# Kernel optimization log

Measured on AMD Instinct MI355X. Metric: run time of the kernel, lower is better.

## Reference

```python
import jax, jax.numpy as jnp
import numpy as np

N_A, N_S, D, H = 100000, 50000, 256, 128
E_AA, E_SS, E_SA = 800000, 400000, 800000


def setup_inputs() -> dict:
    key = jax.random.key(0)
    ks = jax.random.split(key, 13)
    s = 0.05
    return {
        "x_article": jax.random.normal(ks[0], (N_A, D), dtype=jnp.float32),
        "x_software": jax.random.normal(ks[1], (N_S, D), dtype=jnp.float32),
        "ei_aa": jax.random.randint(ks[2], (2, E_AA), 0, N_A, dtype=jnp.int32),
        "ei_ss": jax.random.randint(ks[3], (2, E_SS), 0, N_S, dtype=jnp.int32),
        "sa_src": jax.random.randint(ks[4], (E_SA,), 0, N_S, dtype=jnp.int32),
        "sa_dst": jax.random.randint(ks[5], (E_SA,), 0, N_A, dtype=jnp.int32),
        # GCNConv article->article: weight [D,H], bias [H]
        "W_aa": jax.random.normal(ks[6], (D, H), dtype=jnp.float32) * s,
        "b_aa": jnp.zeros((H,), dtype=jnp.float32),
        # GCNConv software->software
        "W_ss": jax.random.normal(ks[7], (D, H), dtype=jnp.float32) * s,
        "b_ss": jnp.zeros((H,), dtype=jnp.float32),
        # SAGEConv software->article: lin_l (neighbor, with bias), lin_r (root, no bias)
        "W_sa_l": jax.random.normal(ks[8], (D, H), dtype=jnp.float32) * s,
        "b_sa_l": jnp.zeros((H,), dtype=jnp.float32),
        "W_sa_r": jax.random.normal(ks[9], (D, H), dtype=jnp.float32) * s,
    }


def _gcn_conv(x, src, dst, W, b, n):
    # PyG GCNConv: transform, add self-loops (weight 1), symmetric norm, scatter-add
    h = x @ W  # [n, H]
    loops = jnp.arange(n, dtype=src.dtype)
    s = jnp.concatenate([src, loops])
    d = jnp.concatenate([dst, loops])
    w = jnp.ones(s.shape[0], dtype=h.dtype)
    deg = jax.ops.segment_sum(w, d, num_segments=n)  # in-degree incl. self-loop
    dinv = jnp.where(deg > 0, jax.lax.rsqrt(deg), 0.0)
    norm = dinv[s] * dinv[d]  # [E+n]
    out = jax.ops.segment_sum(h[s] * norm[:, None], d, num_segments=n)
    return out + b


def _sage_conv(x_src, x_dst, src, dst, W_l, b_l, W_r, n_dst):
    # PyG SAGEConv (mean aggr): lin_l(mean_neighbors) + lin_r(x_dst)
    msum = jax.ops.segment_sum(x_src[src], dst, num_segments=n_dst)  # [n_dst, D]
    cnt = jax.ops.segment_sum(jnp.ones_like(dst, dtype=x_src.dtype), dst, num_segments=n_dst)
    mean = msum / jnp.maximum(cnt, 1.0)[:, None]
    return mean @ W_l + b_l + x_dst @ W_r


def reference(x_article, x_software, ei_aa, ei_ss, sa_src, sa_dst,
              W_aa, b_aa, W_ss, b_ss, W_sa_l, b_sa_l, W_sa_r):
    gcn_art = _gcn_conv(x_article, ei_aa[0], ei_aa[1], W_aa, b_aa, N_A)
    gcn_soft = _gcn_conv(x_software, ei_ss[0], ei_ss[1], W_ss, b_ss, N_S)
    sage_art = _sage_conv(x_software, x_article, sa_src, sa_dst, W_sa_l, b_sa_l, W_sa_r, N_A)
    # HeteroConv aggr='mean' over relations per dst type, then per-type relu
    art = jax.nn.relu((gcn_art + sage_art) * 0.5)
    soft = jax.nn.relu(gcn_soft)
    return art, soft
```

## Files before the change

kernel.cpp:

```cpp
#include <hip/hip_runtime.h>

typedef short short8 __attribute__((ext_vector_type(8)));
typedef float float4v __attribute__((ext_vector_type(4)));
typedef __bf16 bf16x8 __attribute__((ext_vector_type(8)));

#define NA_ 100000
#define NS_ 50000
#define EAA_ 800000
#define ESS_ 400000
#define ESA_ 800000
#define POOLE_ (EAA_ + ESA_ + ESS_)
#define NNODES_ (NA_ + NA_ + NS_)
#define SCAN_BLOCKS_ 62
#define NPAD_ (SCAN_BLOCKS_ * 4096)

static __device__ __forceinline__ float b2f(short s) {
  unsigned int u = ((unsigned int)(unsigned short)s) << 16;
  return __builtin_bit_cast(float, u);
}
static __device__ __forceinline__ short f2b(float f) {
  unsigned int u = __builtin_bit_cast(unsigned int, f);
  u = u + 0x7FFFu + ((u >> 16) & 1u);
  return (short)(u >> 16);
}

__global__ void cvt_k(const float* __restrict__ x, short* __restrict__ y, int n8) {
  int i = blockIdx.x * 256 + threadIdx.x;
  if (i >= n8) return;
  const float* xp = x + (long)i * 8;
  float4v a0 = *(const float4v*)xp;
  float4v a1 = *(const float4v*)(xp + 4);
  short8 r;
#pragma unroll
  for (int j = 0; j < 4; ++j) {
    r[j] = f2b(a0[j]);
    r[4 + j] = f2b(a1[j]);
  }
  *(short8*)&y[(long)i * 8] = r;
}

__global__ void transpose_all_k(const float* __restrict__ W0, const float* __restrict__ W1,
                                const float* __restrict__ W2, const float* __restrict__ W3,
                                short* __restrict__ T0, short* __restrict__ T1,
                                short* __restrict__ T2, short* __restrict__ T3) {
  int tid = blockIdx.x * 256 + threadIdx.x;
  int which = tid >> 15, r = tid & 32767;
  const float* W = which == 0 ? W0 : which == 1 ? W1 : which == 2 ? W2 : W3;
  short* T = which == 0 ? T0 : which == 1 ? T1 : which == 2 ? T2 : T3;
  int k = r >> 7, n = r & 127;
  T[n * 256 + k] = f2b(W[k * 128 + n]);
}

#define LDN 136
__global__ __launch_bounds__(256) void gemm_k(const short* __restrict__ A,
                                              const short* __restrict__ Wt,
                                              short* __restrict__ C, int M) {
  __shared__ short lds[128 * LDN];
  int tid = threadIdx.x;
  int wave = tid >> 6, lane = tid & 63;
  int l16 = lane & 15, lq = lane >> 4;
  int rowBase = blockIdx.x * 256 + wave * 64;

  float4v acc[4][8];
#pragma unroll
  for (int rt = 0; rt < 4; ++rt)
#pragma unroll
    for (int ct = 0; ct < 8; ++ct) acc[rt][ct] = (float4v){0.f, 0.f, 0.f, 0.f};

  for (int phase = 0; phase < 2; ++phase) {
    int kg = phase * 128;
    __syncthreads();
    for (int idx = tid; idx < 128 * 16; idx += 256) {
      int n = idx >> 4, c = idx & 15;
      *(short8*)&lds[n * LDN + c * 8] = *(const short8*)&Wt[n * 256 + kg + c * 8];
    }
    __syncthreads();
#pragma unroll
    for (int ks = 0; ks < 4; ++ks) {
      int k0 = kg + ks * 32;
      short8 af[4];
#pragma unroll
      for (int rt = 0; rt < 4; ++rt) {
        int row = rowBase + rt * 16 + l16;
        if (row >= M) row = M - 1;
        af[rt] = *(const short8*)&A[(long)row * 256 + k0 + lq * 8];
      }
#pragma unroll
      for (int ct = 0; ct < 8; ++ct) {
        short8 bfg = *(const short8*)&lds[(ct * 16 + l16) * LDN + ks * 32 + lq * 8];
#pragma unroll
        for (int rt = 0; rt < 4; ++rt) {
          acc[rt][ct] = __builtin_amdgcn_mfma_f32_16x16x32_bf16(
              __builtin_bit_cast(bf16x8, af[rt]), __builtin_bit_cast(bf16x8, bfg),
              acc[rt][ct], 0, 0, 0);
        }
      }
    }
  }
#pragma unroll
  for (int rt = 0; rt < 4; ++rt) {
    int r0 = rowBase + rt * 16 + lq * 4;
#pragma unroll
    for (int ct = 0; ct < 8; ++ct) {
      int col = ct * 16 + l16;
#pragma unroll
      for (int r = 0; r < 4; ++r) {
        int row = r0 + r;
        if (row < M) C[(long)row * 128 + col] = f2b(acc[rt][ct][r]);
      }
    }
  }
}

__global__ void count_all_k(const int* __restrict__ dst_aa, const int* __restrict__ sa_dst,
                            const int* __restrict__ dst_ss, int* __restrict__ cnt) {
  int i = blockIdx.x * 256 + threadIdx.x;
  if (i < EAA_) atomicAdd(&cnt[dst_aa[i]], 1);
  else if (i < EAA_ + ESA_) atomicAdd(&cnt[NA_ + sa_dst[i - EAA_]], 1);
  else if (i < POOLE_) atomicAdd(&cnt[2 * NA_ + dst_ss[i - EAA_ - ESA_]], 1);
}

__global__ void scanA_k(const int* __restrict__ in, int* __restrict__ part,
                        int* __restrict__ bsums) {
  __shared__ int lds[256];
  int t = threadIdx.x, b = blockIdx.x;
  int base = b * 4096 + t * 16;
  int v[16];
  int run = 0;
#pragma unroll
  for (int j = 0; j < 16; ++j) {
    int x = (base + j < NNODES_) ? in[base + j] : 0;
    v[j] = run;
    run += x;
  }
  lds[t] = run;
  __syncthreads();
  int incl = run;
  for (int off = 1; off < 256; off <<= 1) {
    int add = (t >= off) ? lds[t - off] : 0;
    __syncthreads();
    lds[t] += add;
    incl = lds[t];
    __syncthreads();
  }
  int excl = incl - run;
#pragma unroll
  for (int j = 0; j < 16; ++j) part[base + j] = v[j] + excl;
  if (t == 255) bsums[b] = incl;
}
__global__ void scanB_k(int* __restrict__ bsums) {
  __shared__ int lds[256];
  int t = threadIdx.x;
  int v = (t < SCAN_BLOCKS_) ? bsums[t] : 0;
  lds[t] = v;
  __syncthreads();
  int incl = v;
  for (int off = 1; off < 256; off <<= 1) {
    int add = (t >= off) ? lds[t - off] : 0;
    __syncthreads();
    lds[t] += add;
    incl = lds[t];
    __syncthreads();
  }
  if (t < SCAN_BLOCKS_) bsums[t] = incl - v;
}
__global__ void scanC_k(const int* __restrict__ part, const int* __restrict__ bsums,
                        int* __restrict__ row_ptr, int* __restrict__ cursor) {
  int t = threadIdx.x, b = blockIdx.x;
  int base = b * 4096 + t * 16;
  int sb = bsums[b];
#pragma unroll
  for (int j = 0; j < 16; ++j) {
    int val = part[base + j] + sb;
    row_ptr[base + j] = val;
    cursor[base + j] = val;
  }
}
__global__ void fill_all_k(const int* __restrict__ src_aa, const int* __restrict__ dst_aa,
                           const int* __restrict__ sa_src, const int* __restrict__ sa_dst,
                           const int* __restrict__ src_ss, const int* __restrict__ dst_ss,
                           int* __restrict__ cursor, int* __restrict__ pool) {
  int i = blockIdx.x * 256 + threadIdx.x;
  int s, node;
  if (i < EAA_) { s = src_aa[i]; node = dst_aa[i]; }
  else if (i < EAA_ + ESA_) { int j = i - EAA_; s = sa_src[j]; node = NA_ + sa_dst[j]; }
  else if (i < POOLE_) { int j = i - EAA_ - ESA_; s = src_ss[j]; node = 2 * NA_ + dst_ss[j]; }
  else return;
  int pos = atomicAdd(&cursor[node], 1);
  pool[pos] = s;
}

__global__ void norms_k(const int* __restrict__ cnt, float* __restrict__ dinv_aa,
                        float* __restrict__ dinv_ss, float* __restrict__ invc_sa) {
  int i = blockIdx.x * 256 + threadIdx.x;
  if (i < NA_) {
    dinv_aa[i] = rsqrtf((float)(cnt[i] + 1));
    invc_sa[i] = 1.0f / fmaxf((float)cnt[NA_ + i], 1.0f);
  }
  if (i < NS_) dinv_ss[i] = rsqrtf((float)(cnt[2 * NA_ + i] + 1));
}

__global__ __launch_bounds__(256) void gather_art_k(
    const short* __restrict__ h_aa, const short* __restrict__ y_sl,
    const short* __restrict__ r_a, const int* __restrict__ pool,
    const int* __restrict__ row_ptr, const float* __restrict__ dinv_aa,
    const float* __restrict__ invc_sa, const float* __restrict__ b_aa,
    const float* __restrict__ b_sal, float* __restrict__ out) {
  int wave = threadIdx.x >> 6, lane = threadIdx.x & 63;
  int d = blockIdx.x * 4 + wave;
  if (d >= NA_) return;
  int c = lane * 2;
  float dd = dinv_aa[d];

  float a0 = 0.f, a1 = 0.f;
  {
    int r0 = row_ptr[d], r1 = row_ptr[d + 1];
    for (int jj = r0; jj < r1; jj += 8) {
      int s[8];
      float m[8];
#pragma unroll
      for (int t = 0; t < 8; ++t) {
        int j = jj + t;
        int jc = (j < r1) ? j : (POOLE_ - 1);
        s[t] = pool[jc];
        m[t] = (j < r1) ? 1.f : 0.f;
      }
      short2 hv[8];
#pragma unroll
      for (int t = 0; t < 8; ++t) hv[t] = *(const short2*)&h_aa[(long)s[t] * 128 + c];
      float wv[8];
#pragma unroll
      for (int t = 0; t < 8; ++t) wv[t] = dinv_aa[s[t]] * m[t];
#pragma unroll
      for (int t = 0; t < 8; ++t) {
        float w = wv[t] * dd;
        a0 += b2f(hv[t].x) * w;
        a1 += b2f(hv[t].y) * w;
      }
    }
  }
  float s0 = 0.f, s1 = 0.f;
  {
    int r0 = row_ptr[NA_ + d], r1 = row_ptr[NA_ + d + 1];
    for (int jj = r0; jj < r1; jj += 8) {
      int s[8];
      float m[8];
#pragma unroll
      for (int t = 0; t < 8; ++t) {
        int j = jj + t;
        int jc = (j < r1) ? j : (POOLE_ - 1);
        s[t] = pool[jc];
        m[t] = (j < r1) ? 1.f : 0.f;
      }
      short2 yv[8];
#pragma unroll
      for (int t = 0; t < 8; ++t) yv[t] = *(const short2*)&y_sl[(long)s[t] * 128 + c];
#pragma unroll
      for (int t = 0; t < 8; ++t) {
        s0 += b2f(yv[t].x) * m[t];
        s1 += b2f(yv[t].y) * m[t];
      }
    }
  }
  float ic = invc_sa[d];
  float d2 = dd * dd;
  short2 hv = *(const short2*)&h_aa[(long)d * 128 + c];
  short2 rv = *(const short2*)&r_a[(long)d * 128 + c];
  float2 ba = *(const float2*)&b_aa[c];
  float2 bl = *(const float2*)&b_sal[c];
  float o0 = 0.5f * ((a0 + b2f(hv.x) * d2 + ba.x) + (s0 * ic + bl.x + b2f(rv.x)));
  float o1 = 0.5f * ((a1 + b2f(hv.y) * d2 + ba.y) + (s1 * ic + bl.y + b2f(rv.y)));
  float2 res = make_float2(fmaxf(o0, 0.f), fmaxf(o1, 0.f));
  *(float2*)&out[(long)d * 128 + c] = res;
}

__global__ __launch_bounds__(256) void gather_soft_k(
    const short* __restrict__ h_ss, const int* __restrict__ pool,
    const int* __restrict__ row_ptr, const float* __restrict__ dinv_ss,
    const float* __restrict__ b_ss, float* __restrict__ out) {
  int wave = threadIdx.x >> 6, lane = threadIdx.x & 63;
  int d = blockIdx.x * 4 + wave;
  if (d >= NS_) return;
  int c = lane * 2;
  float dd = dinv_ss[d];
  float a0 = 0.f, a1 = 0.f;
  int r0 = row_ptr[2 * NA_ + d], r1 = row_ptr[2 * NA_ + d + 1];
  for (int jj = r0; jj < r1; jj += 8) {
    int s[8];
    float m[8];
#pragma unroll
    for (int t = 0; t < 8; ++t) {
      int j = jj + t;
      int jc = (j < r1) ? j : (POOLE_ - 1);
      s[t] = pool[jc];
      m[t] = (j < r1) ? 1.f : 0.f;
    }
    short2 hv[8];
#pragma unroll
    for (int t = 0; t < 8; ++t) hv[t] = *(const short2*)&h_ss[(long)s[t] * 128 + c];
    float wv[8];
#pragma unroll
    for (int t = 0; t < 8; ++t) wv[t] = dinv_ss[s[t]] * m[t];
#pragma unroll
    for (int t = 0; t < 8; ++t) {
      float w = wv[t] * dd;
      a0 += b2f(hv[t].x) * w;
      a1 += b2f(hv[t].y) * w;
    }
  }
  float d2 = dd * dd;
  short2 hv = *(const short2*)&h_ss[(long)d * 128 + c];
  float2 bs = *(const float2*)&b_ss[c];
  float o0 = a0 + b2f(hv.x) * d2 + bs.x;
  float o1 = a1 + b2f(hv.y) * d2 + bs.y;
  float2 res = make_float2(fmaxf(o0, 0.f), fmaxf(o1, 0.f));
  *(float2*)&out[(long)d * 128 + c] = res;
}

extern "C" void kernel_launch(void* const* d_in, const int* in_sizes, int n_in,
                              void* d_out, int out_size, void* d_ws, size_t ws_size,
                              hipStream_t stream) {
  const float* x_a = (const float*)d_in[0];
  const float* x_s = (const float*)d_in[1];
  const int* ei_aa = (const int*)d_in[2];
  const int* ei_ss = (const int*)d_in[3];
  const int* sa_src = (const int*)d_in[4];
  const int* sa_dst = (const int*)d_in[5];
  const float* W_aa = (const float*)d_in[6];
  const float* b_aa = (const float*)d_in[7];
  const float* W_ss = (const float*)d_in[8];
  const float* b_ss = (const float*)d_in[9];
  const float* W_sal = (const float*)d_in[10];
  const float* b_sal = (const float*)d_in[11];
  const float* W_sar = (const float*)d_in[12];

  const int* src_aa = ei_aa;
  const int* dst_aa = ei_aa + EAA_;
  const int* src_ss = ei_ss;
  const int* dst_ss = ei_ss + ESS_;

  char* base = (char*)d_ws;
  size_t off = 0;
  auto alloc = [&](size_t bytes) {
    void* p = base + off;
    off += (bytes + 511) & ~(size_t)511;
    return p;
  };
  short* xb_a = (short*)alloc((size_t)NA_ * 256 * 2);
  short* xb_s = (short*)alloc((size_t)NS_ * 256 * 2);
  short* h_aa = (short*)alloc((size_t)NA_ * 128 * 2);
  short* h_ss = (short*)alloc((size_t)NS_ * 128 * 2);
  short* y_sl = (short*)alloc((size_t)NS_ * 128 * 2);
  short* r_a = (short*)alloc((size_t)NA_ * 128 * 2);
  int* pool = (int*)alloc((size_t)POOLE_ * 4);
  int* cnt_all = (int*)alloc((size_t)NNODES_ * 4);
  int* part = (int*)alloc((size_t)NPAD_ * 4);
  int* row_ptr = (int*)alloc((size_t)NPAD_ * 4);
  int* cursor = (int*)alloc((size_t)NPAD_ * 4);
  int* bsums = (int*)alloc(256 * 4);
  float* dinv_aa = (float*)alloc((size_t)NA_ * 4);
  float* dinv_ss = (float*)alloc((size_t)NS_ * 4);
  float* invc_sa = (float*)alloc((size_t)NA_ * 4);
  short* Wt_aa = (short*)alloc(128 * 256 * 2);
  short* Wt_ss = (short*)alloc(128 * 256 * 2);
  short* Wt_sal = (short*)alloc(128 * 256 * 2);
  short* Wt_sar = (short*)alloc(128 * 256 * 2);

  float* out_art = (float*)d_out;
  float* out_soft = (float*)d_out + (size_t)NA_ * 128;

  int gA = (NA_ + 255) / 256, gS = (NS_ + 255) / 256;

  hipMemsetAsync(cnt_all, 0, (size_t)NNODES_ * 4, stream);
  count_all_k<<<(POOLE_ + 255) / 256, 256, 0, stream>>>(dst_aa, sa_dst, dst_ss, cnt_all);
  scanA_k<<<SCAN_BLOCKS_, 256, 0, stream>>>(cnt_all, part, bsums);
  scanB_k<<<1, 256, 0, stream>>>(bsums);
  scanC_k<<<SCAN_BLOCKS_, 256, 0, stream>>>(part, bsums, row_ptr, cursor);
  fill_all_k<<<(POOLE_ + 255) / 256, 256, 0, stream>>>(src_aa, dst_aa, sa_src, sa_dst, src_ss,
                                                       dst_ss, cursor, pool);
  norms_k<<<(NA_ + 255) / 256, 256, 0, stream>>>(cnt_all, dinv_aa, dinv_ss, invc_sa);

  transpose_all_k<<<512, 256, 0, stream>>>(W_aa, W_ss, W_sal, W_sar, Wt_aa, Wt_ss, Wt_sal,
                                           Wt_sar);
  cvt_k<<<(NA_ * 32 + 255) / 256, 256, 0, stream>>>(x_a, xb_a, NA_ * 32);
  cvt_k<<<(NS_ * 32 + 255) / 256, 256, 0, stream>>>(x_s, xb_s, NS_ * 32);
  gemm_k<<<gA, 256, 0, stream>>>(xb_a, Wt_aa, h_aa, NA_);
  gemm_k<<<gA, 256, 0, stream>>>(xb_a, Wt_sar, r_a, NA_);
  gemm_k<<<gS, 256, 0, stream>>>(xb_s, Wt_ss, h_ss, NS_);
  gemm_k<<<gS, 256, 0, stream>>>(xb_s, Wt_sal, y_sl, NS_);

  gather_art_k<<<(NA_ + 3) / 4, 256, 0, stream>>>(h_aa, y_sl, r_a, pool, row_ptr, dinv_aa,
                                                  invc_sa, b_aa, b_sal, out_art);
  gather_soft_k<<<(NS_ + 3) / 4, 256, 0, stream>>>(h_ss, pool, row_ptr, dinv_ss, b_ss, out_soft);
}
```

Before: 648.4 us.

## Fuse paired GEMMs, precompute edge weights into CSR pool, drop second atomic pass

Each input matrix now goes through one GEMM kernel that computes both weight projections at once, so A is read once per node type instead of twice. CSR construction records each edge's slot from the counting atomic, so the fill pass no longer needs a second atomic cursor. It also stores a precomputed normalization weight next to each source index in an int2 pool. The norm kernel is folded into the scan, and the gather kernels read the weight straight from the pool instead of doing an extra dinv lookup per edge. The cost is a pool twice as large plus a pos array, and a GEMM tile with fewer rows per block.

```diff
diff --git a/kernel.cpp b/kernel.cpp
--- a/kernel.cpp
+++ b/kernel.cpp
@@ -51,45 +51,48 @@
   T[n * 256 + k] = f2b(W[k * 128 + n]);
 }
 
-#define LDN 136
-__global__ __launch_bounds__(256) void gemm_k(const short* __restrict__ A,
-                                              const short* __restrict__ Wt,
-                                              short* __restrict__ C, int M) {
-  __shared__ short lds[128 * LDN];
+#define LDK 72
+__global__ __launch_bounds__(256) void gemm2_k(const short* __restrict__ A,
+                                               const short* __restrict__ Wt0,
+                                               const short* __restrict__ Wt1,
+                                               short* __restrict__ C0,
+                                               short* __restrict__ C1, int M) {
+  __shared__ short lds[256 * LDK];
   int tid = threadIdx.x;
   int wave = tid >> 6, lane = tid & 63;
   int l16 = lane & 15, lq = lane >> 4;
-  int rowBase = blockIdx.x * 256 + wave * 64;
-
-  float4v acc[4][8];
-#pragma unroll
-  for (int rt = 0; rt < 4; ++rt)
-#pragma unroll
-    for (int ct = 0; ct < 8; ++ct) acc[rt][ct] = (float4v){0.f, 0.f, 0.f, 0.f};
-
-  for (int phase = 0; phase < 2; ++phase) {
-    int kg = phase * 128;
-    __syncthreads();
-    for (int idx = tid; idx < 128 * 16; idx += 256) {
-      int n = idx >> 4, c = idx & 15;
-      *(short8*)&lds[n * LDN + c * 8] = *(const short8*)&Wt[n * 256 + kg + c * 8];
-    }
-    __syncthreads();
-#pragma unroll
-    for (int ks = 0; ks < 4; ++ks) {
-      int k0 = kg + ks * 32;
-      short8 af[4];
-#pragma unroll
-      for (int rt = 0; rt < 4; ++rt) {
+  int rowBase = blockIdx.x * 128 + wave * 32;
+
+  float4v acc[2][16];
+#pragma unroll
+  for (int rt = 0; rt < 2; ++rt)
+#pragma unroll
+    for (int ct = 0; ct < 16; ++ct) acc[rt][ct] = (float4v){0.f, 0.f, 0.f, 0.f};
+
+  for (int p = 0; p < 4; ++p) {
+    int kp = p * 64;
+    __syncthreads();
+    for (int idx = tid; idx < 2048; idx += 256) {
+      int row = idx >> 3, c = idx & 7;
+      const short* Wsrc = (row < 128) ? &Wt0[row * 256] : &Wt1[(row - 128) * 256];
+      *(short8*)&lds[row * LDK + c * 8] = *(const short8*)&Wsrc[kp + c * 8];
+    }
+    __syncthreads();
+#pragma unroll
+    for (int ks = 0; ks < 2; ++ks) {
+      int k0 = kp + ks * 32;
+      short8 af[2];
+#pragma unroll
+      for (int rt = 0; rt < 2; ++rt) {
         int row = rowBase + rt * 16 + l16;
         if (row >= M) row = M - 1;
         af[rt] = *(const short8*)&A[(long)row * 256 + k0 + lq * 8];
       }
 #pragma unroll
-      for (int ct = 0; ct < 8; ++ct) {
-        short8 bfg = *(const short8*)&lds[(ct * 16 + l16) * LDN + ks * 32 + lq * 8];
-#pragma unroll
-        for (int rt = 0; rt < 4; ++rt) {
+      for (int ct = 0; ct < 16; ++ct) {
+        short8 bfg = *(const short8*)&lds[(ct * 16 + l16) * LDK + ks * 32 + lq * 8];
+#pragma unroll
+        for (int rt = 0; rt < 2; ++rt) {
           acc[rt][ct] = __builtin_amdgcn_mfma_f32_16x16x32_bf16(
               __builtin_bit_cast(bf16x8, af[rt]), __builtin_bit_cast(bf16x8, bfg),
               acc[rt][ct], 0, 0, 0);
@@ -98,11 +101,12 @@
     }
   }
 #pragma unroll
-  for (int rt = 0; rt < 4; ++rt) {
+  for (int rt = 0; rt < 2; ++rt) {
     int r0 = rowBase + rt * 16 + lq * 4;
 #pragma unroll
-    for (int ct = 0; ct < 8; ++ct) {
-      int col = ct * 16 + l16;
+    for (int ct = 0; ct < 16; ++ct) {
+      short* C = (ct < 8) ? C0 : C1;
+      int col = (ct & 7) * 16 + l16;
 #pragma unroll
       for (int r = 0; r < 4; ++r) {
         int row = r0 + r;
@@ -112,12 +116,16 @@
   }
 }
 
-__global__ void count_all_k(const int* __restrict__ dst_aa, const int* __restrict__ sa_dst,
-                            const int* __restrict__ dst_ss, int* __restrict__ cnt) {
+__global__ void count_pos_k(const int* __restrict__ dst_aa, const int* __restrict__ sa_dst,
+                            const int* __restrict__ dst_ss, int* __restrict__ cnt,
+                            int* __restrict__ pos) {
   int i = blockIdx.x * 256 + threadIdx.x;
-  if (i < EAA_) atomicAdd(&cnt[dst_aa[i]], 1);
-  else if (i < EAA_ + ESA_) atomicAdd(&cnt[NA_ + sa_dst[i - EAA_]], 1);
-  else if (i < POOLE_) atomicAdd(&cnt[2 * NA_ + dst_ss[i - EAA_ - ESA_]], 1);
+  int node;
+  if (i < EAA_) node = dst_aa[i];
+  else if (i < EAA_ + ESA_) node = NA_ + sa_dst[i - EAA_];
+  else if (i < POOLE_) node = 2 * NA_ + dst_ss[i - EAA_ - ESA_];
+  else return;
+  pos[i] = atomicAdd(&cnt[node], 1);
 }
 
 __global__ void scanA_k(const int* __restrict__ in, int* __restrict__ part,
@@ -165,75 +173,83 @@
   if (t < SCAN_BLOCKS_) bsums[t] = incl - v;
 }
 __global__ void scanC_k(const int* __restrict__ part, const int* __restrict__ bsums,
-                        int* __restrict__ row_ptr, int* __restrict__ cursor) {
+                        const int* __restrict__ cnt, int* __restrict__ row_ptr,
+                        float* __restrict__ dinv_aa, float* __restrict__ dinv_ss,
+                        float* __restrict__ invc_sa) {
   int t = threadIdx.x, b = blockIdx.x;
   int base = b * 4096 + t * 16;
   int sb = bsums[b];
 #pragma unroll
   for (int j = 0; j < 16; ++j) {
-    int val = part[base + j] + sb;
-    row_ptr[base + j] = val;
-    cursor[base + j] = val;
-  }
-}
-__global__ void fill_all_k(const int* __restrict__ src_aa, const int* __restrict__ dst_aa,
-                           const int* __restrict__ sa_src, const int* __restrict__ sa_dst,
-                           const int* __restrict__ src_ss, const int* __restrict__ dst_ss,
-                           int* __restrict__ cursor, int* __restrict__ pool) {
+    int i = base + j;
+    row_ptr[i] = part[i] + sb;
+    if (i < NA_) dinv_aa[i] = rsqrtf((float)(cnt[i] + 1));
+    else if (i < 2 * NA_) invc_sa[i - NA_] = 1.0f / fmaxf((float)cnt[i], 1.0f);
+    else if (i < NNODES_) dinv_ss[i - 2 * NA_] = rsqrtf((float)(cnt[i] + 1));
+  }
+}
+
+__global__ void fill2_k(const int* __restrict__ src_aa, const int* __restrict__ dst_aa,
+                        const int* __restrict__ sa_src, const int* __restrict__ sa_dst,
+                        const int* __restrict__ src_ss, const int* __restrict__ dst_ss,
+                        const int* __restrict__ row_ptr, const int* __restrict__ pos,
+                        const float* __restrict__ dinv_aa, const float* __restrict__ dinv_ss,
+                        const float* __restrict__ invc_sa, int2* __restrict__ pool) {
   int i = blockIdx.x * 256 + threadIdx.x;
   int s, node;
-  if (i < EAA_) { s = src_aa[i]; node = dst_aa[i]; }
-  else if (i < EAA_ + ESA_) { int j = i - EAA_; s = sa_src[j]; node = NA_ + sa_dst[j]; }
-  else if (i < POOLE_) { int j = i - EAA_ - ESA_; s = src_ss[j]; node = 2 * NA_ + dst_ss[j]; }
-  else return;
-  int pos = atomicAdd(&cursor[node], 1);
-  pool[pos] = s;
-}
-
-__global__ void norms_k(const int* __restrict__ cnt, float* __restrict__ dinv_aa,
-                        float* __restrict__ dinv_ss, float* __restrict__ invc_sa) {
-  int i = blockIdx.x * 256 + threadIdx.x;
-  if (i < NA_) {
-    dinv_aa[i] = rsqrtf((float)(cnt[i] + 1));
-    invc_sa[i] = 1.0f / fmaxf((float)cnt[NA_ + i], 1.0f);
-  }
-  if (i < NS_) dinv_ss[i] = rsqrtf((float)(cnt[2 * NA_ + i] + 1));
+  float w;
+  if (i < EAA_) {
+    s = src_aa[i];
+    int d = dst_aa[i];
+    node = d;
+    w = dinv_aa[s] * dinv_aa[d];
+  } else if (i < EAA_ + ESA_) {
+    int j = i - EAA_;
+    s = sa_src[j];
+    int d = sa_dst[j];
+    node = NA_ + d;
+    w = invc_sa[d];
+  } else if (i < POOLE_) {
+    int j = i - EAA_ - ESA_;
+    s = src_ss[j];
+    int d = dst_ss[j];
+    node = 2 * NA_ + d;
+    w = dinv_ss[s] * dinv_ss[d];
+  } else
+    return;
+  pool[row_ptr[node] + pos[i]] = make_int2(s, __builtin_bit_cast(int, w));
 }
 
 __global__ __launch_bounds__(256) void gather_art_k(
     const short* __restrict__ h_aa, const short* __restrict__ y_sl,
-    const short* __restrict__ r_a, const int* __restrict__ pool,
+    const short* __restrict__ r_a, const int2* __restrict__ pool,
     const int* __restrict__ row_ptr, const float* __restrict__ dinv_aa,
-    const float* __restrict__ invc_sa, const float* __restrict__ b_aa,
-    const float* __restrict__ b_sal, float* __restrict__ out) {
+    const float* __restrict__ b_aa, const float* __restrict__ b_sal,
+    float* __restrict__ out) {
   int wave = threadIdx.x >> 6, lane = threadIdx.x & 63;
   int d = blockIdx.x * 4 + wave;
   if (d >= NA_) return;
   int c = lane * 2;
-  float dd = dinv_aa[d];
 
   float a0 = 0.f, a1 = 0.f;
   {
     int r0 = row_ptr[d], r1 = row_ptr[d + 1];
     for (int jj = r0; jj < r1; jj += 8) {
-      int s[8];
+      int2 pv[8];
       float m[8];
 #pragma unroll
       for (int t = 0; t < 8; ++t) {
         int j = jj + t;
         int jc = (j < r1) ? j : (POOLE_ - 1);
-        s[t] = pool[jc];
+        pv[t] = pool[jc];
         m[t] = (j < r1) ? 1.f : 0.f;
       }
       short2 hv[8];
 #pragma unroll
-      for (int t = 0; t < 8; ++t) hv[t] = *(const short2*)&h_aa[(long)s[t] * 128 + c];
-      float wv[8];
-#pragma unroll
-      for (int t = 0; t < 8; ++t) wv[t] = dinv_aa[s[t]] * m[t];
+      for (int t = 0; t < 8; ++t) hv[t] = *(const short2*)&h_aa[(long)pv[t].x * 128 + c];
 #pragma unroll
       for (int t = 0; t < 8; ++t) {
-        float w = wv[t] * dd;
+        float w = __builtin_bit_cast(float, pv[t].y) * m[t];
         a0 += b2f(hv[t].x) * w;
         a1 += b2f(hv[t].y) * w;
       }
@@ -243,71 +259,69 @@
   {
     int r0 = row_ptr[NA_ + d], r1 = row_ptr[NA_ + d + 1];
     for (int jj = r0; jj < r1; jj += 8) {
-      int s[8];
+      int2 pv[8];
       float m[8];
 #pragma unroll
       for (int t = 0; t < 8; ++t) {
         int j = jj + t;
         int jc = (j < r1) ? j : (POOLE_ - 1);
-        s[t] = pool[jc];
+        pv[t] = pool[jc];
         m[t] = (j < r1) ? 1.f : 0.f;
       }
       short2 yv[8];
 #pragma unroll
-      for (int t = 0; t < 8; ++t) yv[t] = *(const short2*)&y_sl[(long)s[t] * 128 + c];
+      for (int t = 0; t < 8; ++t) yv[t] = *(const short2*)&y_sl[(long)pv[t].x * 128 + c];
 #pragma unroll
       for (int t = 0; t < 8; ++t) {
-        s0 += b2f(yv[t].x) * m[t];
-        s1 += b2f(yv[t].y) * m[t];
-      }
-    }
-  }
-  float ic = invc_sa[d];
+        float w = __builtin_bit_cast(float, pv[t].y) * m[t];
+        s0 += b2f(yv[t].x) * w;
+        s1 += b2f(yv[t].y) * w;
+      }
+    }
+  }
+  float dd = dinv_aa[d];
   float d2 = dd * dd;
   short2 hv = *(const short2*)&h_aa[(long)d * 128 + c];
   short2 rv = *(const short2*)&r_a[(long)d * 128 + c];
   float2 ba = *(const float2*)&b_aa[c];
   float2 bl = *(const float2*)&b_sal[c];
-  float o0 = 0.5f * ((a0 + b2f(hv.x) * d2 + ba.x) + (s0 * ic + bl.x + b2f(rv.x)));
-  float o1 = 0.5f * ((a1 + b2f(hv.y) * d2 + ba.y) + (s1 * ic + bl.y + b2f(rv.y)));
+  float o0 = 0.5f * ((a0 + b2f(hv.x) * d2 + ba.x) + (s0 + bl.x + b2f(rv.x)));
+  float o1 = 0.5f * ((a1 + b2f(hv.y) * d2 + ba.y) + (s1 + bl.y + b2f(rv.y)));
   float2 res = make_float2(fmaxf(o0, 0.f), fmaxf(o1, 0.f));
   *(float2*)&out[(long)d * 128 + c] = res;
 }
 
 __global__ __launch_bounds__(256) void gather_soft_k(
-    const short* __restrict__ h_ss, const int* __restrict__ pool,
+    const short* __restrict__ h_ss, const int2* __restrict__ pool,
     const int* __restrict__ row_ptr, const float* __restrict__ dinv_ss,
     const float* __restrict__ b_ss, float* __restrict__ out) {
   int wave = threadIdx.x >> 6, lane = threadIdx.x & 63;
   int d = blockIdx.x * 4 + wave;
   if (d >= NS_) return;
   int c = lane * 2;
-  float dd = dinv_ss[d];
   float a0 = 0.f, a1 = 0.f;
   int r0 = row_ptr[2 * NA_ + d], r1 = row_ptr[2 * NA_ + d + 1];
   for (int jj = r0; jj < r1; jj += 8) {
-    int s[8];
+    int2 pv[8];
     float m[8];
 #pragma unroll
     for (int t = 0; t < 8; ++t) {
       int j = jj + t;
       int jc = (j < r1) ? j : (POOLE_ - 1);
-      s[t] = pool[jc];
+      pv[t] = pool[jc];
       m[t] = (j < r1) ? 1.f : 0.f;
     }
     short2 hv[8];
 #pragma unroll
-    for (int t = 0; t < 8; ++t) hv[t] = *(const short2*)&h_ss[(long)s[t] * 128 + c];
-    float wv[8];
-#pragma unroll
-    for (int t = 0; t < 8; ++t) wv[t] = dinv_ss[s[t]] * m[t];
+    for (int t = 0; t < 8; ++t) hv[t] = *(const short2*)&h_ss[(long)pv[t].x * 128 + c];
 #pragma unroll
     for (int t = 0; t < 8; ++t) {
-      float w = wv[t] * dd;
+      float w = __builtin_bit_cast(float, pv[t].y) * m[t];
       a0 += b2f(hv[t].x) * w;
       a1 += b2f(hv[t].y) * w;
     }
   }
+  float dd = dinv_ss[d];
   float d2 = dd * dd;
   short2 hv = *(const short2*)&h_ss[(long)d * 128 + c];
   float2 bs = *(const float2*)&b_ss[c];
@@ -352,11 +366,11 @@
   short* h_ss = (short*)alloc((size_t)NS_ * 128 * 2);
   short* y_sl = (short*)alloc((size_t)NS_ * 128 * 2);
   short* r_a = (short*)alloc((size_t)NA_ * 128 * 2);
-  int* pool = (int*)alloc((size_t)POOLE_ * 4);
+  int2* pool = (int2*)alloc((size_t)POOLE_ * 8);
+  int* pos = (int*)alloc((size_t)POOLE_ * 4);
   int* cnt_all = (int*)alloc((size_t)NNODES_ * 4);
   int* part = (int*)alloc((size_t)NPAD_ * 4);
   int* row_ptr = (int*)alloc((size_t)NPAD_ * 4);
-  int* cursor = (int*)alloc((size_t)NPAD_ * 4);
   int* bsums = (int*)alloc(256 * 4);
   float* dinv_aa = (float*)alloc((size_t)NA_ * 4);
   float* dinv_ss = (float*)alloc((size_t)NS_ * 4);
@@ -369,27 +383,24 @@
   float* out_art = (float*)d_out;
   float* out_soft = (float*)d_out + (size_t)NA_ * 128;
 
-  int gA = (NA_ + 255) / 256, gS = (NS_ + 255) / 256;
-
   hipMemsetAsync(cnt_all, 0, (size_t)NNODES_ * 4, stream);
-  count_all_k<<<(POOLE_ + 255) / 256, 256, 0, stream>>>(dst_aa, sa_dst, dst_ss, cnt_all);
+  count_pos_k<<<(POOLE_ + 255) / 256, 256, 0, stream>>>(dst_aa, sa_dst, dst_ss, cnt_all, pos);
   scanA_k<<<SCAN_BLOCKS_, 256, 0, stream>>>(cnt_all, part, bsums);
   scanB_k<<<1, 256, 0, stream>>>(bsums);
-  scanC_k<<<SCAN_BLOCKS_, 256, 0, stream>>>(part, bsums, row_ptr, cursor);
-  fill_all_k<<<(POOLE_ + 255) / 256, 256, 0, stream>>>(src_aa, dst_aa, sa_src, sa_dst, src_ss,
-                                                       dst_ss, cursor, pool);
-  norms_k<<<(NA_ + 255) / 256, 256, 0, stream>>>(cnt_all, dinv_aa, dinv_ss, invc_sa);
+  scanC_k<<<SCAN_BLOCKS_, 256, 0, stream>>>(part, bsums, cnt_all, row_ptr, dinv_aa, dinv_ss,
+                                            invc_sa);
+  fill2_k<<<(POOLE_ + 255) / 256, 256, 0, stream>>>(src_aa, dst_aa, sa_src, sa_dst, src_ss,
+                                                    dst_ss, row_ptr, pos, dinv_aa, dinv_ss,
+                                                    invc_sa, pool);
 
   transpose_all_k<<<512, 256, 0, stream>>>(W_aa, W_ss, W_sal, W_sar, Wt_aa, Wt_ss, Wt_sal,
                                            Wt_sar);
   cvt_k<<<(NA_ * 32 + 255) / 256, 256, 0, stream>>>(x_a, xb_a, NA_ * 32);
   cvt_k<<<(NS_ * 32 + 255) / 256, 256, 0, stream>>>(x_s, xb_s, NS_ * 32);
-  gemm_k<<<gA, 256, 0, stream>>>(xb_a, Wt_aa, h_aa, NA_);
-  gemm_k<<<gA, 256, 0, stream>>>(xb_a, Wt_sar, r_a, NA_);
-  gemm_k<<<gS, 256, 0, stream>>>(xb_s, Wt_ss, h_ss, NS_);
-  gemm_k<<<gS, 256, 0, stream>>>(xb_s, Wt_sal, y_sl, NS_);
+  gemm2_k<<<(NA_ + 127) / 128, 256, 0, stream>>>(xb_a, Wt_aa, Wt_sar, h_aa, r_a, NA_);
+  gemm2_k<<<(NS_ + 127) / 128, 256, 0, stream>>>(xb_s, Wt_ss, Wt_sal, h_ss, y_sl, NS_);
 
   gather_art_k<<<(NA_ + 3) / 4, 256, 0, stream>>>(h_aa, y_sl, r_a, pool, row_ptr, dinv_aa,
-                                                  invc_sa, b_aa, b_sal, out_art);
+                                                  b_aa, b_sal, out_art);
   gather_soft_k<<<(NS_ + 3) / 4, 256, 0, stream>>>(h_ss, pool, row_ptr, dinv_ss, b_ss, out_soft);
 }
```

After: 640.6 us. Within noise of the previous version (-1.2%).
